# Kernel optimization log

Hardware: AMD Instinct MI355X
Metric: run time of the kernel (lower is better)

Reference implementation:

```python
import jax, jax.numpy as jnp
import numpy as np

D, H, G, HD = 2048, 16, 4, 128  # d_model, num_heads, num_groups, head_dim
B, S = 2, 2048


def _rope(x):
    # x: [B, heads, S, HD]; RoPE with concat(freqs, freqs) layout (rotate_half style)
    seq = x.shape[2]
    inv_freq = 1.0 / (10000.0 ** (jnp.arange(0, HD, 2, dtype=jnp.float32) / HD))  # [HD/2]
    t = jnp.arange(seq, dtype=jnp.float32)
    freqs = t[:, None] * inv_freq[None, :]              # [S, HD/2]
    emb = jnp.concatenate([freqs, freqs], axis=-1)      # [S, HD]
    cos = jnp.cos(emb)[None, None]                      # [1,1,S,HD]
    sin = jnp.sin(emb)[None, None]
    x1, x2 = jnp.split(x, 2, axis=-1)
    rot = jnp.concatenate([-x2, x1], axis=-1)           # rotate_half
    return x * cos + rot * sin


def setup_inputs() -> dict:
    key = jax.random.key(0)
    ks = jax.random.split(key, 5)
    x = jax.random.normal(ks[0], (B, S, D), dtype=jnp.float32)
    # weights stored as [in, out] so y = x @ W (equivalent to torch Linear with W^T)
    Wq = jax.random.normal(ks[1], (D, D), dtype=jnp.float32) * 0.02
    Wk = jax.random.normal(ks[2], (D, G * HD), dtype=jnp.float32) * 0.02
    Wv = jax.random.normal(ks[3], (D, G * HD), dtype=jnp.float32) * 0.02
    Wo = jax.random.normal(ks[4], (D, D), dtype=jnp.float32) * 0.02
    # causal mask: True = masked (matches torch masked_fill semantics)
    mask = ~jnp.tril(jnp.ones((S, S), dtype=bool))[None, None]  # [1,1,S,S]
    return {"x": x, "Wq": Wq, "Wk": Wk, "Wv": Wv, "Wo": Wo, "mask": mask}


def reference(x, Wq, Wk, Wv, Wo, mask):
    b, s, _ = x.shape
    q = (x @ Wq).reshape(b, s, H, HD).transpose(0, 2, 1, 3)   # [B,H,S,HD]
    k = (x @ Wk).reshape(b, s, G, HD).transpose(0, 2, 1, 3)   # [B,G,S,HD]
    v = (x @ Wv).reshape(b, s, G, HD).transpose(0, 2, 1, 3)   # [B,G,S,HD]
    q = _rope(q)
    k = _rope(k)
    # GQA: repeat_interleave KV groups across heads
    k = jnp.repeat(k, H // G, axis=1)                         # [B,H,S,HD]
    v = jnp.repeat(v, H // G, axis=1)
    scale = jnp.float32(1.0 / np.sqrt(HD))
    scores = jnp.einsum('bhqd,bhkd->bhqk', q, k) * scale      # [B,H,S,S]
    scores = jnp.where(mask, jnp.float32(-1e9), scores)
    attn = jax.nn.softmax(scores, axis=-1)
    ctx = jnp.einsum('bhqk,bhkd->bhqd', attn, v)              # [B,H,S,HD]
    ctx = ctx.transpose(0, 2, 1, 3).reshape(b, s, D)
    return ctx @ Wo
```

## Files before the change

### kernel.cpp

```cpp
#include <hip/hip_runtime.h>
#include <hip/hip_bf16.h>
#include <math.h>

#define BB 2
#define SS 2048
#define DD 2048
#define HH 16
#define GG 4
#define HDIM 128
#define DKV (GG * HDIM)
#define MS (BB * SS)
#define QKVS 3072

typedef __attribute__((ext_vector_type(8))) short bf16x8;
typedef __attribute__((ext_vector_type(4))) float f32x4;
typedef __attribute__((ext_vector_type(4))) unsigned int u32x4;

__device__ __forceinline__ ushort f2bf(float x) {
    __hip_bfloat16 b = __float2bfloat16(x);
    return *(ushort*)&b;
}
__device__ __forceinline__ float bf2f(ushort u) {
    __hip_bfloat16 b;
    *(ushort*)&b = u;
    return __bfloat162float(b);
}

#define GLOAD_LDS(src, dst)                                                        \
    __builtin_amdgcn_global_load_lds(                                              \
        (const __attribute__((address_space(1))) unsigned int*)(src),              \
        (__attribute__((address_space(3))) unsigned int*)(dst), 16, 0, 0)

#define WAITV(n) asm volatile("s_waitcnt vmcnt(" #n ")" ::: "memory")

__global__ void cast_bf16(const float* __restrict__ X, ushort* __restrict__ O, int total8) {
    int idx = blockIdx.x * blockDim.x + threadIdx.x;
    if (idx >= total8) return;
    const float4* p = (const float4*)X + (size_t)idx * 2;
    float4 a = p[0], b = p[1];
    float v[8] = {a.x, a.y, a.z, a.w, b.x, b.y, b.z, b.w};
    ushort r[8];
#pragma unroll
    for (int j = 0; j < 8; ++j) r[j] = f2bf(v[j]);
    *((u32x4*)O + idx) = *(u32x4*)r;
}

__global__ __launch_bounds__(256) void transpose_cast(const float* __restrict__ W,
                                                      ushort* __restrict__ WT,
                                                      int K, int N) {
    __shared__ ushort tile[32][33];
    const int tx = threadIdx.x & 31, ty = threadIdx.x >> 5;
    const int n0 = blockIdx.x * 32, k0 = blockIdx.y * 32;
#pragma unroll
    for (int i = 0; i < 4; ++i)
        tile[ty + i * 8][tx] = f2bf(W[(size_t)(k0 + ty + i * 8) * N + n0 + tx]);
    __syncthreads();
#pragma unroll
    for (int i = 0; i < 4; ++i)
        WT[(size_t)(n0 + ty + i * 8) * K + k0 + tx] = tile[tx][ty + i * 8];
}

__global__ __launch_bounds__(256) void transpose_v(const ushort* __restrict__ QKV,
                                                   ushort* __restrict__ VT) {
    __shared__ ushort tile[32][33];
    const int tx = threadIdx.x & 31, ty = threadIdx.x >> 5;
    const int d0 = blockIdx.x * 32;
    const int k0 = blockIdx.y * 32;
    const int b = blockIdx.z;
#pragma unroll
    for (int i = 0; i < 4; ++i)
        tile[ty + i * 8][tx] =
            QKV[(size_t)(b * SS + k0 + ty + i * 8) * QKVS + 2560 + d0 + tx];
    __syncthreads();
    const int posl = ((tx & 12) << 1) | ((tx & 16) >> 2) | (tx & 3);
#pragma unroll
    for (int i = 0; i < 4; ++i)
        VT[((size_t)b * DKV + d0 + ty + i * 8) * SS + k0 + posl] = tile[tx][ty + i * 8];
}

template <int BM, bool OUT_BF16>
__global__ __launch_bounds__(512) void gemm8(const ushort* __restrict__ A,
                                             const ushort* __restrict__ BT,
                                             void* __restrict__ Cout,
                                             int M, int N, int K) {
    constexpr int ABUF = BM * 32;
    constexpr int BBUF = 256 * 32;
    constexpr int MFR = BM / 32;
    constexpr int NPH = MFR / 4;
    __shared__ ushort As[4 * ABUF];
    __shared__ ushort Bs[4 * BBUF];

    const int t = threadIdx.x;
    const int w = t >> 6, l = t & 63;
    const int lm = l & 15, lw = l >> 4;
    const int wr = w >> 2, wc = w & 3;
    const int nx = gridDim.x;
    const int bid = blockIdx.y * nx + blockIdx.x;
    const int cpx = (nx * gridDim.y) >> 3;
    const int swb = (bid & 7) * cpx + (bid >> 3);
    const int bm = (swb / nx) * BM, bn = (swb % nx) * 256;

    const int NT = K >> 5;
    const int swzc = (lw ^ ((lm >> 1) & 3)) * 8;

    const int ar0 = t >> 2, ac0 = ((t & 3) ^ ((ar0 >> 1) & 3));
    const ushort* a0 = A + (size_t)(bm + ar0) * K + ac0 * 8;
    const int ar1 = (t + 512) >> 2, ac1 = (((t + 512) & 3) ^ ((ar1 >> 1) & 3));
    const ushort* a1 = A + (size_t)(bm + ar1) * K + ac1 * 8;
    const int br0 = t >> 2, bc0 = ((t & 3) ^ ((br0 >> 1) & 3));
    const ushort* b0 = BT + (size_t)(bn + br0) * K + bc0 * 8;
    const int br1 = (t + 512) >> 2, bc1 = (((t + 512) & 3) ^ ((br1 >> 1) & 3));
    const ushort* b1 = BT + (size_t)(bn + br1) * K + bc1 * 8;

    auto STAGE = [&](int kt) {
        const int buf = kt & 3;
        GLOAD_LDS(a0, &As[buf * ABUF + t * 8]);
        a0 += 32;
        if constexpr (BM == 256) {
            GLOAD_LDS(a1, &As[buf * ABUF + (t + 512) * 8]);
            a1 += 32;
        }
        GLOAD_LDS(b0, &Bs[buf * BBUF + t * 8]);
        b0 += 32;
        GLOAD_LDS(b1, &Bs[buf * BBUF + (t + 512) * 8]);
        b1 += 32;
    };

    f32x4 acc[MFR][4];
#pragma unroll
    for (int m = 0; m < MFR; ++m)
#pragma unroll
        for (int n = 0; n < 4; ++n) acc[m][n] = (f32x4){0.f, 0.f, 0.f, 0.f};

    STAGE(0);
    STAGE(1);

#pragma unroll 1
    for (int kt = 0; kt < NT; ++kt) {
        if (kt + 2 < NT) {
            STAGE(kt + 2);
            if constexpr (BM == 256) WAITV(8); else WAITV(6);
        } else if (kt + 1 < NT) {
            if constexpr (BM == 256) WAITV(4); else WAITV(3);
        } else {
            WAITV(0);
        }
        __builtin_amdgcn_s_barrier();

        const ushort* Ab = &As[(kt & 3) * ABUF];
        const ushort* Bb = &Bs[(kt & 3) * BBUF];
        bf16x8 bfr[4];
#pragma unroll
        for (int n = 0; n < 4; ++n)
            bfr[n] = *(const bf16x8*)&Bb[(wc * 64 + n * 16 + lm) * 32 + swzc];
#pragma unroll
        for (int ph = 0; ph < NPH; ++ph) {
            bf16x8 af[4];
#pragma unroll
            for (int i = 0; i < 4; ++i)
                af[i] = *(const bf16x8*)&Ab[(wr * (BM / 2) + (ph * 4 + i) * 16 + lm) * 32 + swzc];
            __builtin_amdgcn_s_setprio(1);
#pragma unroll
            for (int i = 0; i < 4; ++i)
#pragma unroll
                for (int n = 0; n < 4; ++n)
                    acc[ph * 4 + i][n] =
                        __builtin_amdgcn_mfma_f32_16x16x32_bf16(af[i], bfr[n], acc[ph * 4 + i][n], 0, 0, 0);
            __builtin_amdgcn_s_setprio(0);
        }
    }

#pragma unroll
    for (int m = 0; m < MFR; ++m)
#pragma unroll
        for (int n = 0; n < 4; ++n)
#pragma unroll
            for (int r = 0; r < 4; ++r) {
                int row = bm + wr * (BM / 2) + m * 16 + lw * 4 + r;
                int col = bn + wc * 64 + n * 16 + lm;
                if (OUT_BF16)
                    ((ushort*)Cout)[(size_t)row * N + col] = f2bf(acc[m][n][r]);
                else
                    ((float*)Cout)[(size_t)row * N + col] = acc[m][n][r];
            }
}

__global__ void rope_bf16(ushort* __restrict__ X, int nheads, int colOff, int total) {
    int idx = blockIdx.x * blockDim.x + threadIdx.x;
    if (idx >= total) return;
    int i = idx & 63;
    int hh = (idx >> 6) % nheads;
    int row = idx / (64 * nheads);
    int s = row & (SS - 1);
    float inv = exp2f((float)i * -0.2076205059304601f);
    float ang = (float)s * inv;
    float c, sn;
    __sincosf(ang, &sn, &c);
    size_t base = (size_t)row * QKVS + colOff + (size_t)hh * HDIM + i;
    float x1 = bf2f(X[base]), x2 = bf2f(X[base + 64]);
    X[base] = f2bf(x1 * c - x2 * sn);
    X[base + 64] = f2bf(x2 * c + x1 * sn);
}

#define SCL 0.08838834764831845f
#define CEXP 0.1275296340545927f
#define THRRAW 90.50966799187809f

__global__ __launch_bounds__(512) void attn_mfma(const ushort* __restrict__ QKV,
                                                 const ushort* __restrict__ VT,
                                                 ushort* __restrict__ Ctx) {
    __shared__ ushort Ks[2][64 * 128];
    __shared__ ushort Vs[2][128 * 64];
    const int t = threadIdx.x;
    const int w = t >> 6;
    const int l = t & 63;
    const int lm = l & 15, lw = l >> 4;
    const int bid = blockIdx.x;
    const int g = bid & 3;
    const int b = (bid >> 2) & 1;
    const int within = bid >> 3;
    const int xq = within & 7;
    const int h = g * 4 + (within >> 3);
    const int swz = (lm & 7) << 3;

    const ushort* kbase = QKV + (size_t)(b * SS) * QKVS + 2048 + g * HDIM;
    const ushort* vbase = VT + ((size_t)b * DKV + g * HDIM) * SS;

    const short one_bf = (short)0x3F80;
    const bf16x8 ones = {one_bf, one_bf, one_bf, one_bf, one_bf, one_bf, one_bf, one_bf};

    const int kr0 = t >> 4, ko0 = t & 15;
    const int kr1 = (t + 512) >> 4, ko1 = (t + 512) & 15;
    const int vr0 = t >> 3, vo0 = t & 7;
    const int vr1 = (t + 512) >> 3, vo1 = (t + 512) & 7;
    ushort* kd0a = &Ks[0][t * 8];
    ushort* kd0b = &Ks[1][t * 8];
    ushort* kd1a = &Ks[0][(t + 512) * 8];
    ushort* kd1b = &Ks[1][(t + 512) * 8];
    ushort* vd0a = &Vs[0][t * 8];
    ushort* vd0b = &Vs[1][t * 8];
    ushort* vd1a = &Vs[0][(t + 512) * 8];
    ushort* vd1b = &Vs[1][(t + 512) * 8];

#pragma unroll 1
    for (int phase = 0; phase < 2; ++phase) {
        const int qt = (phase == 0) ? xq : (15 - xq);
        const int q0 = qt * 128;
        const int qw = q0 + w * 16;
        const int q = qw + lm;
        const int ntiles = 2 * qt + 2;
        const int lt = (qw + 15) >> 6;

        const ushort* ks0 = kbase + (size_t)kr0 * QKVS + ((ko0 ^ (kr0 & 7)) * 8);
        const ushort* ks1 = kbase + (size_t)kr1 * QKVS + ((ko1 ^ (kr1 & 7)) * 8);
        const ushort* vs0 = vbase + (size_t)vr0 * SS + ((vo0 ^ (vr0 & 7)) * 8);
        const ushort* vs1 = vbase + (size_t)vr1 * SS + ((vo1 ^ (vr1 & 7)) * 8);

        bf16x8 qa[4];
        {
            const ushort* qp = QKV + (size_t)(b * SS + qw + lm) * QKVS + h * HDIM + lw * 8;
#pragma unroll
            for (int kk = 0; kk < 4; ++kk)
                qa[kk] = *(const bf16x8*)(qp + kk * 32);
        }

        f32x4 acc[8];
#pragma unroll
        for (int d = 0; d < 8; ++d) acc[d] = (f32x4){0.f, 0.f, 0.f, 0.f};
        f32x4 accl = (f32x4){0.f, 0.f, 0.f, 0.f};
        float m = -INFINITY;

        GLOAD_LDS(ks0, kd0a);
        GLOAD_LDS(ks1, kd1a);
        ks0 += 64 * QKVS;
        ks1 += 64 * QKVS;
        GLOAD_LDS(vs0, vd0a);
        GLOAD_LDS(vs1, vd1a);
        vs0 += 64;
        vs1 += 64;
        asm volatile("s_waitcnt vmcnt(0)" ::: "memory");
        __builtin_amdgcn_s_barrier();

#pragma unroll 1
        for (int tile = 0; tile < ntiles; ++tile) {
            const int cur = tile & 1;
            const int kv0 = tile * 64;
            const bool more = (tile + 1 < ntiles);
            if (more) {
                GLOAD_LDS(ks0, cur ? kd0a : kd0b);
                GLOAD_LDS(ks1, cur ? kd1a : kd1b);
                ks0 += 64 * QKVS;
                ks1 += 64 * QKVS;
                GLOAD_LDS(vs0, cur ? vd0a : vd0b);
                GLOAD_LDS(vs1, cur ? vd1a : vd1b);
                vs0 += 64;
                vs1 += 64;
            }

            if (tile <= lt) {
                f32x4 sfT[4];
#pragma unroll
                for (int kvb = 0; kvb < 4; ++kvb) sfT[kvb] = (f32x4){0.f, 0.f, 0.f, 0.f};
                __builtin_amdgcn_s_setprio(1);
#pragma unroll
                for (int kvb = 0; kvb < 4; ++kvb)
#pragma unroll
                    for (int kk = 0; kk < 4; ++kk) {
                        bf16x8 kb = *(const bf16x8*)&Ks[cur][(kvb * 16 + lm) * 128 + ((kk * 32 + lw * 8) ^ swz)];
                        sfT[kvb] = __builtin_amdgcn_mfma_f32_16x16x32_bf16(kb, qa[kk], sfT[kvb], 0, 0, 0);
                    }
                __builtin_amdgcn_s_setprio(0);

                if (tile == lt) {
#pragma unroll
                    for (int kvb = 0; kvb < 4; ++kvb)
#pragma unroll
                        for (int r = 0; r < 4; ++r) {
                            int kv = kv0 + kvb * 16 + lw * 4 + r;
                            if (kv > q) sfT[kvb][r] = -INFINITY;
                        }
                }

                float rm = fmaxf(fmaxf(sfT[0][0], sfT[0][1]), fmaxf(sfT[0][2], sfT[0][3]));
#pragma unroll
                for (int kvb = 1; kvb < 4; ++kvb) {
                    rm = fmaxf(rm, fmaxf(fmaxf(sfT[kvb][0], sfT[kvb][1]),
                                         fmaxf(sfT[kvb][2], sfT[kvb][3])));
                }
                rm = fmaxf(rm, __shfl_xor(rm, 16));
                rm = fmaxf(rm, __shfl_xor(rm, 32));

                bool stable = (rm - m <= THRRAW);
                if (!__all((int)stable)) {
                    float mn = fmaxf(m, rm);
                    float alpha_l = exp2f((m - mn) * CEXP);
                    m = mn;
                    float ar[4];
#pragma unroll
                    for (int r = 0; r < 4; ++r)
                        ar[r] = __shfl(alpha_l, (l & 48) | (lw * 4 + r));
#pragma unroll
                    for (int d = 0; d < 8; ++d) {
                        acc[d][0] *= ar[0];
                        acc[d][1] *= ar[1];
                        acc[d][2] *= ar[2];
                        acc[d][3] *= ar[3];
                    }
                    accl[0] *= ar[0];
                    accl[1] *= ar[1];
                    accl[2] *= ar[2];
                    accl[3] *= ar[3];
                }

                bf16x8 pa[2];
                float mC = m * CEXP;
#pragma unroll
                for (int kvb = 0; kvb < 4; ++kvb)
#pragma unroll
                    for (int r = 0; r < 4; ++r) {
                        float pv = exp2f(fmaf(sfT[kvb][r], CEXP, -mC));
                        pa[kvb >> 1][(kvb & 1) * 4 + r] = (short)f2bf(pv);
                    }

                __builtin_amdgcn_s_setprio(1);
#pragma unroll
                for (int kks = 0; kks < 2; ++kks) {
                    accl = __builtin_amdgcn_mfma_f32_16x16x32_bf16(pa[kks], ones, accl, 0, 0, 0);
#pragma unroll
                    for (int dcol = 0; dcol < 8; ++dcol) {
                        bf16x8 vb = *(const bf16x8*)&Vs[cur][(dcol * 16 + lm) * 64 + ((kks * 32 + lw * 8) ^ swz)];
                        acc[dcol] = __builtin_amdgcn_mfma_f32_16x16x32_bf16(pa[kks], vb, acc[dcol], 0, 0, 0);
                    }
                }
                __builtin_amdgcn_s_setprio(0);
            }

            if (more) {
                asm volatile("s_waitcnt vmcnt(0)" ::: "memory");
                __builtin_amdgcn_s_barrier();
            }
        }

        float rinv[4];
#pragma unroll
        for (int r = 0; r < 4; ++r) rinv[r] = 1.f / accl[r];
        ushort* cp = Ctx + (size_t)(b * SS + qw) * DD + h * HDIM;
#pragma unroll
        for (int d = 0; d < 8; ++d)
#pragma unroll
            for (int r = 0; r < 4; ++r)
                cp[(size_t)(lw * 4 + r) * DD + d * 16 + lm] = f2bf(acc[d][r] * rinv[r]);
        __builtin_amdgcn_s_barrier();
    }
}

extern "C" void kernel_launch(void* const* d_in, const int* in_sizes, int n_in,
                              void* d_out, int out_size, void* d_ws, size_t ws_size,
                              hipStream_t stream) {
    const float* x  = (const float*)d_in[0];
    const float* Wq = (const float*)d_in[1];
    const float* Wk = (const float*)d_in[2];
    const float* Wv = (const float*)d_in[3];
    const float* Wo = (const float*)d_in[4];
    float* out = (float*)d_out;

    ushort* xh    = (ushort*)d_ws;
    ushort* QKV   = xh + (size_t)MS * DD;
    ushort* VTb   = QKV + (size_t)MS * QKVS;
    ushort* WqkvT = VTb + (size_t)MS * DKV;
    ushort* WoT   = WqkvT + (size_t)QKVS * DD;
    ushort* Ch    = xh;

    dim3 blk(256);
    int nx8 = MS * DD / 8;
    cast_bf16<<<(nx8 + 255) / 256, 256, 0, stream>>>(x, xh, nx8);

    transpose_cast<<<dim3(DD / 32, DD / 32), blk, 0, stream>>>(Wq, WqkvT, DD, DD);
    transpose_cast<<<dim3(DKV / 32, DD / 32), blk, 0, stream>>>(Wk, WqkvT + (size_t)DD * DD, DD, DKV);
    transpose_cast<<<dim3(DKV / 32, DD / 32), blk, 0, stream>>>(Wv, WqkvT + (size_t)(DD + DKV) * DD, DD, DKV);

    gemm8<256, true><<<dim3(QKVS / 256, MS / 256), dim3(512), 0, stream>>>(xh, WqkvT, QKV, MS, QKVS, DD);

    int nq = MS * HH * 64;
    rope_bf16<<<(nq + 255) / 256, 256, 0, stream>>>(QKV, HH, 0, nq);
    int nk = MS * GG * 64;
    rope_bf16<<<(nk + 255) / 256, 256, 0, stream>>>(QKV, GG, 2048, nk);

    transpose_v<<<dim3(DKV / 32, SS / 32, BB), blk, 0, stream>>>(QKV, VTb);

    attn_mfma<<<dim3(256), dim3(512), 0, stream>>>(QKV, VTb, Ch);

    transpose_cast<<<dim3(DD / 32, DD / 32), blk, 0, stream>>>(Wo, WoT, DD, DD);
    gemm8<128, false><<<dim3(DD / 256, MS / 128), dim3(512), 0, stream>>>(Ch, WoT, out, MS, DD, DD);
}
```

Measured before the change: 216.6 us.

## Retile GEMMs to BM=128 with 3-stage LDS ring, merge RoPE launches

The GEMM kernel now fixes the M tile at 128 and templates the N tile (256 for QKV, 128 for the output projection). It moves from a 4-slot to a 3-slot LDS ring, issuing the next prefetch after the barrier rather than before the wait. This doubles the block count for both GEMMs to improve occupancy and CU coverage, and cuts LDS use, at the cost of less reuse per block. The two RoPE launches for Q and K are also merged into one kernel covering all 20 heads, saving a launch.

Result: faster. 210.4 us (-2.9%).

```diff
diff --git a/kernel.cpp b/kernel.cpp
--- a/kernel.cpp
+++ b/kernel.cpp
@@ -78,52 +78,49 @@
         VT[((size_t)b * DKV + d0 + ty + i * 8) * SS + k0 + posl] = tile[tx][ty + i * 8];
 }
 
-template <int BM, bool OUT_BF16>
+template <int BN, bool OUT_BF16>
 __global__ __launch_bounds__(512) void gemm8(const ushort* __restrict__ A,
                                              const ushort* __restrict__ BT,
                                              void* __restrict__ Cout,
                                              int M, int N, int K) {
-    constexpr int ABUF = BM * 32;
-    constexpr int BBUF = 256 * 32;
-    constexpr int MFR = BM / 32;
-    constexpr int NPH = MFR / 4;
-    __shared__ ushort As[4 * ABUF];
-    __shared__ ushort Bs[4 * BBUF];
+    constexpr int ABUF = 128 * 32;
+    constexpr int BBUF = BN * 32;
+    constexpr int NWC = BN / 64;
+    constexpr int NWM = 8 / NWC;
+    constexpr int ROWS = 128 / NWM;
+    constexpr int MFR = ROWS / 16;
+    __shared__ ushort As[3 * ABUF];
+    __shared__ ushort Bs[3 * BBUF];
 
     const int t = threadIdx.x;
     const int w = t >> 6, l = t & 63;
     const int lm = l & 15, lw = l >> 4;
-    const int wr = w >> 2, wc = w & 3;
+    const int wr = w / NWC, wc = w % NWC;
     const int nx = gridDim.x;
     const int bid = blockIdx.y * nx + blockIdx.x;
     const int cpx = (nx * gridDim.y) >> 3;
     const int swb = (bid & 7) * cpx + (bid >> 3);
-    const int bm = (swb / nx) * BM, bn = (swb % nx) * 256;
+    const int bm = (swb / nx) * 128, bn = (swb % nx) * BN;
 
     const int NT = K >> 5;
     const int swzc = (lw ^ ((lm >> 1) & 3)) * 8;
 
-    const int ar0 = t >> 2, ac0 = ((t & 3) ^ ((ar0 >> 1) & 3));
+    const int ar0 = t >> 2, ac0 = (t & 3) ^ ((ar0 >> 1) & 3);
     const ushort* a0 = A + (size_t)(bm + ar0) * K + ac0 * 8;
-    const int ar1 = (t + 512) >> 2, ac1 = (((t + 512) & 3) ^ ((ar1 >> 1) & 3));
-    const ushort* a1 = A + (size_t)(bm + ar1) * K + ac1 * 8;
-    const int br0 = t >> 2, bc0 = ((t & 3) ^ ((br0 >> 1) & 3));
+    const int br0 = t >> 2, bc0 = (t & 3) ^ ((br0 >> 1) & 3);
     const ushort* b0 = BT + (size_t)(bn + br0) * K + bc0 * 8;
-    const int br1 = (t + 512) >> 2, bc1 = (((t + 512) & 3) ^ ((br1 >> 1) & 3));
+    const int br1 = (t + 512) >> 2, bc1 = ((t + 512) & 3) ^ ((br1 >> 1) & 3);
     const ushort* b1 = BT + (size_t)(bn + br1) * K + bc1 * 8;
 
-    auto STAGE = [&](int kt) {
-        const int buf = kt & 3;
-        GLOAD_LDS(a0, &As[buf * ABUF + t * 8]);
+    auto STAGE = [&](int slot) {
+        GLOAD_LDS(a0, &As[slot * ABUF + t * 8]);
         a0 += 32;
-        if constexpr (BM == 256) {
-            GLOAD_LDS(a1, &As[buf * ABUF + (t + 512) * 8]);
-            a1 += 32;
+        GLOAD_LDS(b0, &Bs[slot * BBUF + t * 8]);
+        b0 += 32;
+        if constexpr (BN == 256) {
+            GLOAD_LDS(b1, &Bs[slot * BBUF + (t + 512) * 8]);
+            b1 += 32;
         }
-        GLOAD_LDS(b0, &Bs[buf * BBUF + t * 8]);
-        b0 += 32;
-        GLOAD_LDS(b1, &Bs[buf * BBUF + (t + 512) * 8]);
-        b1 += 32;
     };
 
     f32x4 acc[MFR][4];
@@ -134,40 +131,37 @@
 
     STAGE(0);
     STAGE(1);
+    int cs = 0, ps = 2;
 
 #pragma unroll 1
     for (int kt = 0; kt < NT; ++kt) {
-        if (kt + 2 < NT) {
-            STAGE(kt + 2);
-            if constexpr (BM == 256) WAITV(8); else WAITV(6);
-        } else if (kt + 1 < NT) {
-            if constexpr (BM == 256) WAITV(4); else WAITV(3);
+        if (kt + 1 < NT) {
+            if constexpr (BN == 256) WAITV(3); else WAITV(2);
         } else {
             WAITV(0);
         }
         __builtin_amdgcn_s_barrier();
-
-        const ushort* Ab = &As[(kt & 3) * ABUF];
-        const ushort* Bb = &Bs[(kt & 3) * BBUF];
-        bf16x8 bfr[4];
+        if (kt + 2 < NT) STAGE(ps);
+
+        const ushort* Ab = &As[cs * ABUF];
+        const ushort* Bb = &Bs[cs * BBUF];
+        bf16x8 bfr[4], af[MFR];
 #pragma unroll
         for (int n = 0; n < 4; ++n)
             bfr[n] = *(const bf16x8*)&Bb[(wc * 64 + n * 16 + lm) * 32 + swzc];
 #pragma unroll
-        for (int ph = 0; ph < NPH; ++ph) {
-            bf16x8 af[4];
-#pragma unroll
-            for (int i = 0; i < 4; ++i)
-                af[i] = *(const bf16x8*)&Ab[(wr * (BM / 2) + (ph * 4 + i) * 16 + lm) * 32 + swzc];
-            __builtin_amdgcn_s_setprio(1);
-#pragma unroll
-            for (int i = 0; i < 4; ++i)
-#pragma unroll
-                for (int n = 0; n < 4; ++n)
-                    acc[ph * 4 + i][n] =
-                        __builtin_amdgcn_mfma_f32_16x16x32_bf16(af[i], bfr[n], acc[ph * 4 + i][n], 0, 0, 0);
-            __builtin_amdgcn_s_setprio(0);
-        }
+        for (int i = 0; i < MFR; ++i)
+            af[i] = *(const bf16x8*)&Ab[(wr * ROWS + i * 16 + lm) * 32 + swzc];
+        __builtin_amdgcn_s_setprio(1);
+#pragma unroll
+        for (int i = 0; i < MFR; ++i)
+#pragma unroll
+            for (int n = 0; n < 4; ++n)
+                acc[i][n] = __builtin_amdgcn_mfma_f32_16x16x32_bf16(af[i], bfr[n], acc[i][n], 0, 0, 0);
+        __builtin_amdgcn_s_setprio(0);
+
+        cs = (cs == 2) ? 0 : cs + 1;
+        ps = (ps == 2) ? 0 : ps + 1;
     }
 
 #pragma unroll
@@ -176,7 +170,7 @@
         for (int n = 0; n < 4; ++n)
 #pragma unroll
             for (int r = 0; r < 4; ++r) {
-                int row = bm + wr * (BM / 2) + m * 16 + lw * 4 + r;
+                int row = bm + wr * ROWS + m * 16 + lw * 4 + r;
                 int col = bn + wc * 64 + n * 16 + lm;
                 if (OUT_BF16)
                     ((ushort*)Cout)[(size_t)row * N + col] = f2bf(acc[m][n][r]);
@@ -185,18 +179,19 @@
             }
 }
 
-__global__ void rope_bf16(ushort* __restrict__ X, int nheads, int colOff, int total) {
+__global__ void rope_bf16(ushort* __restrict__ X, int total) {
     int idx = blockIdx.x * blockDim.x + threadIdx.x;
     if (idx >= total) return;
     int i = idx & 63;
-    int hh = (idx >> 6) % nheads;
-    int row = idx / (64 * nheads);
+    int hh = (idx >> 6) % 20;
+    int row = idx / (64 * 20);
     int s = row & (SS - 1);
+    int colOff = (hh < 16) ? hh * HDIM : 2048 + (hh - 16) * HDIM;
     float inv = exp2f((float)i * -0.2076205059304601f);
     float ang = (float)s * inv;
     float c, sn;
     __sincosf(ang, &sn, &c);
-    size_t base = (size_t)row * QKVS + colOff + (size_t)hh * HDIM + i;
+    size_t base = (size_t)row * QKVS + colOff + i;
     float x1 = bf2f(X[base]), x2 = bf2f(X[base + 64]);
     X[base] = f2bf(x1 * c - x2 * sn);
     X[base + 64] = f2bf(x2 * c + x1 * sn);
@@ -419,17 +414,15 @@
     transpose_cast<<<dim3(DKV / 32, DD / 32), blk, 0, stream>>>(Wk, WqkvT + (size_t)DD * DD, DD, DKV);
     transpose_cast<<<dim3(DKV / 32, DD / 32), blk, 0, stream>>>(Wv, WqkvT + (size_t)(DD + DKV) * DD, DD, DKV);
 
-    gemm8<256, true><<<dim3(QKVS / 256, MS / 256), dim3(512), 0, stream>>>(xh, WqkvT, QKV, MS, QKVS, DD);
-
-    int nq = MS * HH * 64;
-    rope_bf16<<<(nq + 255) / 256, 256, 0, stream>>>(QKV, HH, 0, nq);
-    int nk = MS * GG * 64;
-    rope_bf16<<<(nk + 255) / 256, 256, 0, stream>>>(QKV, GG, 2048, nk);
+    gemm8<256, true><<<dim3(QKVS / 256, MS / 128), dim3(512), 0, stream>>>(xh, WqkvT, QKV, MS, QKVS, DD);
+
+    int nrope = MS * 20 * 64;
+    rope_bf16<<<(nrope + 255) / 256, 256, 0, stream>>>(QKV, nrope);
 
     transpose_v<<<dim3(DKV / 32, SS / 32, BB), blk, 0, stream>>>(QKV, VTb);
 
     attn_mfma<<<dim3(256), dim3(512), 0, stream>>>(QKV, VTb, Ch);
 
     transpose_cast<<<dim3(DD / 32, DD / 32), blk, 0, stream>>>(Wo, WoT, DD, DD);
-    gemm8<128, false><<<dim3(DD / 256, MS / 128), dim3(512), 0, stream>>>(Ch, WoT, out, MS, DD, DD);
-}
+    gemm8<128, false><<<dim3(DD / 128, MS / 128), dim3(512), 0, stream>>>(Ch, WoT, out, MS, DD, DD);
+}
```
